# Kernel optimization log

Measured on AMD Instinct MI355X. Metric: run time of the kernel, lower is better.

The kernel has to match this reference:

```python
import jax, jax.numpy as jnp
import numpy as np

K_NEIGHBORS = 3  # self.K in DSVDD


def setup_inputs() -> dict:
    key = jax.random.key(0)
    k1, k2 = jax.random.split(key)
    B, N, C = 16, 3136, 112   # batch, h*w patches, descriptor channels
    M = 3136                  # memory-bank size
    phi_p = jax.random.normal(k1, (B, N, C), dtype=jnp.float32)
    C_bank = jax.random.normal(k2, (C, M), dtype=jnp.float32)
    return {"phi_p": phi_p, "C_bank": C_bank, "h": 56}


def reference(phi_p, C_bank, h):
    # squared distances via ||phi||^2 + ||c||^2 - 2 phi.c  -> (B, N, M)
    features = jnp.sum(phi_p * phi_p, axis=2, keepdims=True)        # (B, N, 1)
    centers = jnp.sum(C_bank * C_bank, axis=0, keepdims=True)       # (1, M)
    f_c = 2.0 * jnp.einsum('bnc,cm->bnm', phi_p, C_bank)            # (B, N, M)
    dist = jnp.sqrt(features + centers - f_c)                        # (B, N, M)
    # K smallest distances (ascending, like torch.topk(largest=False))
    neg_topk, _ = jax.lax.top_k(-dist, K_NEIGHBORS)                  # (B, N, K)
    dist_k = -neg_topk
    # softmin over K, take weight of the nearest neighbor times its distance
    softmin0 = jax.nn.softmax(-dist_k, axis=-1)[:, :, 0]             # (B, N)
    score = softmin0 * dist_k[:, :, 0]                               # (B, N)
    B, N = score.shape
    w = N // h
    return score.reshape(B, 1, h, w)  # b c h w with c=1
```

## Files before the change

kernel.cpp:

```cpp
#include <hip/hip_runtime.h>
#include <stdint.h>


typedef short s16x8 __attribute__((ext_vector_type(8)));
typedef float fx4 __attribute__((ext_vector_type(4)));

#define M_TOT 3136
#define CC 112
#define NROWS 50176
#define N_TILES_TOT 50

__device__ __forceinline__ unsigned short f2bf(float x) {
  unsigned u = __float_as_uint(x);
  u += 0x7fffu + ((u >> 16) & 1u);
  return (unsigned short)(u >> 16);
}

__device__ __forceinline__ void async16(const void* g, void* l) {
  __builtin_amdgcn_global_load_lds(
      (const __attribute__((address_space(1))) unsigned int*)g,
      (__attribute__((address_space(3))) unsigned int*)l, 16, 0, 0);
}

#define INSERT3(T0, T1, T2, V)                                  \
  do {                                                          \
    const float _a0 = (T0), _a1 = (T1), _v = (V);               \
    (T0) = fmaxf(_a0, _v);                                      \
    (T1) = __builtin_amdgcn_fmed3f(_a0, _a1, _v);               \
    (T2) = __builtin_amdgcn_fmed3f(_a1, (T2), _v);              \
  } while (0)

__global__ __launch_bounds__(256) void dsvdd_prep0(const float* __restrict__ Cb,
                                                   float* __restrict__ c2g) {
  const int m = blockIdx.x * 256 + threadIdx.x;
  if (m >= 3200) return;
  float ss = 20000.0f;
  if (m < M_TOT) {
    ss = 0.f;
    for (int k = 0; k < CC; ++k) {
      const float x = Cb[(size_t)k * M_TOT + m];
      ss += x * x;
    }
  }
  c2g[m] = ss;
}

__global__ __launch_bounds__(256) void dsvdd_prep1(const float* __restrict__ Cb,
                                                   const float* __restrict__ c2g,
                                                   unsigned char* __restrict__ CT2) {
  const int tile = blockIdx.x;
#pragma unroll
  for (int it = 0; it < 4; ++it) {
    const int s = it * 256 + threadIdx.x;
    const int f = s >> 8;
    const int ks = (s >> 6) & 3;
    const int l = s & 63;
    const int mm = tile * 64 + f * 16 + (l & 15);
    const bool mv = (mm < M_TOT);
    const int k0 = ks * 32 + (l >> 4) * 8;
    float v[8];
#pragma unroll
    for (int j = 0; j < 8; ++j) {
      const int k = k0 + j;
      float x = 0.f;
      if (k < CC) x = mv ? Cb[(size_t)k * M_TOT + mm] : 0.f;
      else if (k < 116) x = -0.125f * c2g[mm];
      v[j] = x;
    }
    uint4 pk;
    pk.x = (unsigned)f2bf(v[0]) | ((unsigned)f2bf(v[1]) << 16);
    pk.y = (unsigned)f2bf(v[2]) | ((unsigned)f2bf(v[3]) << 16);
    pk.z = (unsigned)f2bf(v[4]) | ((unsigned)f2bf(v[5]) << 16);
    pk.w = (unsigned)f2bf(v[6]) | ((unsigned)f2bf(v[7]) << 16);
    *(uint4*)(CT2 + (size_t)tile * 16384 + (size_t)s * 16) = pk;
  }
}

__global__ __launch_bounds__(256, 2) void dsvdd_stage1(const float* __restrict__ phi,
                                                       const unsigned char* __restrict__ CT2,
                                                       float* __restrict__ part,
                                                       float* __restrict__ featg, int nT) {
  __shared__ __align__(16) unsigned char lds[49152];

  const int t = threadIdx.x;
  const int lane = t & 63;
  const int w = t >> 6;
  const int g = w >> 1;
  const int h = w & 1;
  const int cq = lane & 15;
  const int kq = lane >> 4;
  const int c = blockIdx.y;
  const int tile0 = c * nT;
  const long rowBase = (long)blockIdx.x * 128;

#define STAGE(OFF, TIDX)                                                          \
  do {                                                                            \
    const unsigned char* _g =                                                     \
        CT2 + (size_t)(TIDX)*16384 + (size_t)w * 4096 + (size_t)lane * 16;        \
    unsigned char* _l = lds + (OFF) + w * 4096;                                   \
    _Pragma("unroll") for (int ii = 0; ii < 4; ++ii)                              \
        async16(_g + ii * 1024, _l + ii * 1024);                                  \
  } while (0)

  s16x8 bg[4][4];
  float ssr[4];
#pragma unroll
  for (int pf = 0; pf < 4; ++pf) {
    ssr[pf] = 0.f;
    const float* rp = phi + (size_t)(rowBase + g * 64 + pf * 16 + cq) * CC;
#pragma unroll
    for (int ks = 0; ks < 4; ++ks) {
      const int k0 = ks * 32 + kq * 8;
      s16x8 v;
      if (k0 <= 104) {
        const float4 a = *(const float4*)(rp + k0);
        const float4 b = *(const float4*)(rp + k0 + 4);
        ssr[pf] += a.x * a.x + a.y * a.y + a.z * a.z + a.w * a.w;
        ssr[pf] += b.x * b.x + b.y * b.y + b.z * b.z + b.w * b.w;
        v[0] = (short)f2bf(a.x); v[1] = (short)f2bf(a.y);
        v[2] = (short)f2bf(a.z); v[3] = (short)f2bf(a.w);
        v[4] = (short)f2bf(b.x); v[5] = (short)f2bf(b.y);
        v[6] = (short)f2bf(b.z); v[7] = (short)f2bf(b.w);
      } else if (k0 == 112) {
        v[0] = v[1] = v[2] = v[3] = (short)0x3f80;
        v[4] = v[5] = v[6] = v[7] = 0;
      } else {
        v = (s16x8)0;
      }
      bg[ks][pf] = v;
    }
    ssr[pf] += __shfl_xor(ssr[pf], 16);
    ssr[pf] += __shfl_xor(ssr[pf], 32);
  }

  STAGE(0, tile0 + 0);
  STAGE(16384, tile0 + 1);

  if (c == 0 && kq == 0) {
#pragma unroll
    for (int pf = 0; pf < 4; ++pf)
      featg[rowBase + g * 64 + pf * 16 + cq] = ssr[pf];
  }

  float t0[4], t1[4], t2[4];
#pragma unroll
  for (int pf = 0; pf < 4; ++pf) t0[pf] = t1[pf] = t2[pf] = -3.0e38f;

  int rd_off = 0;
  for (int tt = 0; tt < nT; ++tt) {
    if (tt + 1 < nT) {
      asm volatile("s_waitcnt vmcnt(4)" ::: "memory");
    } else {
      asm volatile("s_waitcnt vmcnt(0)" ::: "memory");
    }
    __builtin_amdgcn_s_barrier();
    __builtin_amdgcn_sched_barrier(0);
    if (tt + 2 < nT) {
      int wr = rd_off + 32768;
      if (wr >= 49152) wr -= 49152;
      STAGE(wr, tile0 + tt + 2);
    }
    const unsigned char* rd = lds + rd_off;
#pragma unroll
    for (int mf = 0; mf < 2; ++mf) {
      const int f = h * 2 + mf;
      s16x8 af[4];
#pragma unroll
      for (int ks = 0; ks < 4; ++ks)
        af[ks] = *(const s16x8*)(rd + (f * 4 + ks) * 1024 + lane * 16);
      fx4 acc[4];
      const fx4 zz = {0.f, 0.f, 0.f, 0.f};
#pragma unroll
      for (int ks = 0; ks < 4; ++ks)
#pragma unroll
        for (int pf = 0; pf < 4; ++pf)
          acc[pf] = __builtin_amdgcn_mfma_f32_16x16x32_bf16(
              af[ks], bg[ks][pf], (ks == 0) ? zz : acc[pf], 0, 0, 0);
#pragma unroll
      for (int pf = 0; pf < 4; ++pf)
#pragma unroll
        for (int rg = 0; rg < 4; ++rg)
          INSERT3(t0[pf], t1[pf], t2[pf], acc[pf][rg]);
    }
    rd_off += 16384;
    if (rd_off == 49152) rd_off = 0;
  }
#undef STAGE

#pragma unroll
  for (int pf = 0; pf < 4; ++pf) {
#pragma unroll
    for (int off = 16; off < 64; off <<= 1) {
      const float b0 = __shfl_xor(t0[pf], off);
      const float b1 = __shfl_xor(t1[pf], off);
      const float b2 = __shfl_xor(t2[pf], off);
      INSERT3(t0[pf], t1[pf], t2[pf], b0);
      INSERT3(t0[pf], t1[pf], t2[pf], b1);
      INSERT3(t0[pf], t1[pf], t2[pf], b2);
    }
  }
  __syncthreads();
  float(*const mg)[8] = (float(*)[8])lds;
  if (kq == 0) {
#pragma unroll
    for (int pf = 0; pf < 4; ++pf) {
      const int row = g * 64 + pf * 16 + cq;
      mg[row][h * 3 + 0] = t0[pf];
      mg[row][h * 3 + 1] = t1[pf];
      mg[row][h * 3 + 2] = t2[pf];
    }
  }
  __syncthreads();
  if (t < 128) {
    float s0 = mg[t][0], s1 = mg[t][1], s2 = mg[t][2];
    INSERT3(s0, s1, s2, mg[t][3]);
    INSERT3(s0, s1, s2, mg[t][4]);
    INSERT3(s0, s1, s2, mg[t][5]);
    float* dst = part + ((size_t)c * NROWS + rowBase + t) * 3;
    dst[0] = s0; dst[1] = s1; dst[2] = s2;
  }
}

__global__ __launch_bounds__(256) void dsvdd_stage2(const float* __restrict__ part,
                                                    const float* __restrict__ featg,
                                                    float* __restrict__ out, int S) {
  const int row = blockIdx.x * 256 + threadIdx.x;
  if (row >= NROWS) return;
  float s0 = -3.0e38f, s1 = -3.0e38f, s2 = -3.0e38f;
  for (int c = 0; c < S; ++c) {
    const float* p = part + ((size_t)c * NROWS + row) * 3;
    INSERT3(s0, s1, s2, p[0]);
    INSERT3(s0, s1, s2, p[1]);
    INSERT3(s0, s1, s2, p[2]);
  }
  const float feat = featg[row];
  const float d0 = sqrtf(fmaxf(feat - 2.f * s0, 0.f));
  const float d1 = sqrtf(fmaxf(feat - 2.f * s1, 0.f));
  const float d2 = sqrtf(fmaxf(feat - 2.f * s2, 0.f));
  const float w0 = 1.0f / (1.0f + __expf(d0 - d1) + __expf(d0 - d2));
  out[row] = w0 * d0;
}

extern "C" void kernel_launch(void* const* d_in, const int* in_sizes, int n_in,
                              void* d_out, int out_size, void* d_ws, size_t ws_size,
                              hipStream_t stream) {
  (void)in_sizes; (void)n_in; (void)out_size;
  const float* phi = (const float*)d_in[0];
  const float* Cb = (const float*)d_in[1];
  float* out = (float*)d_out;
  unsigned char* CT2 = (unsigned char*)d_ws;
  float* c2g = (float*)((unsigned char*)d_ws + 819200);
  float* featg = (float*)((unsigned char*)d_ws + 832000);
  float* partp = (float*)((unsigned char*)d_ws + 832000 + 200704);
  const size_t base = 832000 + 200704;
  int S = 1;
  if (ws_size >= base + (size_t)5 * NROWS * 12) S = 5;
  else if (ws_size >= base + (size_t)2 * NROWS * 12) S = 2;
  const int nT = N_TILES_TOT / S;
  dsvdd_prep0<<<13, 256, 0, stream>>>(Cb, c2g);
  dsvdd_prep1<<<50, 256, 0, stream>>>(Cb, c2g, CT2);
  dsvdd_stage1<<<dim3(392, S), 256, 0, stream>>>(phi, CT2, partp, featg, nT);
  dsvdd_stage2<<<196, 256, 0, stream>>>(partp, featg, out, S);
}
```

Baseline: 76.65 us.

## Load bank tiles directly to registers and fuse prep kernels

Removes the LDS triple-buffered async staging of bank tiles and instead has each wave load its A fragments straight from global memory into registers, double-buffered across iterations, with no barriers. The two prep kernels are merged into one that computes the column norms with an in-block reduction, and the feature-norm computation is skipped for non-zero splits. This drops the block-wide barrier per tile and cuts LDS use, which could raise occupancy. In exchange it relies on L2/L1 for reuse of the shared tile across the four waves and adds register pressure.

```diff
diff --git a/kernel.cpp b/kernel.cpp
--- a/kernel.cpp
+++ b/kernel.cpp
@@ -14,12 +14,6 @@
   unsigned u = __float_as_uint(x);
   u += 0x7fffu + ((u >> 16) & 1u);
   return (unsigned short)(u >> 16);
-}
-
-__device__ __forceinline__ void async16(const void* g, void* l) {
-  __builtin_amdgcn_global_load_lds(
-      (const __attribute__((address_space(1))) unsigned int*)g,
-      (__attribute__((address_space(3))) unsigned int*)l, 16, 0, 0);
 }
 
 #define INSERT3(T0, T1, T2, V)                                  \
@@ -30,32 +24,36 @@
     (T2) = __builtin_amdgcn_fmed3f(_a1, (T2), _v);              \
   } while (0)
 
-__global__ __launch_bounds__(256) void dsvdd_prep0(const float* __restrict__ Cb,
-                                                   float* __restrict__ c2g) {
-  const int m = blockIdx.x * 256 + threadIdx.x;
-  if (m >= 3200) return;
-  float ss = 20000.0f;
+__global__ __launch_bounds__(256) void dsvdd_prep(const float* __restrict__ Cb,
+                                                  unsigned char* __restrict__ CT2) {
+  const int tile = blockIdx.x;
+  __shared__ float partial[256];
+  __shared__ float c2s[64];
+  const int tm = threadIdx.x & 63;
+  const int seg = threadIdx.x >> 6;
+  const int m = tile * 64 + tm;
+  float ss = 0.f;
   if (m < M_TOT) {
-    ss = 0.f;
-    for (int k = 0; k < CC; ++k) {
+    for (int k = seg * 28; k < seg * 28 + 28; ++k) {
       const float x = Cb[(size_t)k * M_TOT + m];
       ss += x * x;
     }
   }
-  c2g[m] = ss;
-}
-
-__global__ __launch_bounds__(256) void dsvdd_prep1(const float* __restrict__ Cb,
-                                                   const float* __restrict__ c2g,
-                                                   unsigned char* __restrict__ CT2) {
-  const int tile = blockIdx.x;
+  partial[threadIdx.x] = ss;
+  __syncthreads();
+  if (seg == 0) {
+    const float c2 = partial[tm] + partial[64 + tm] + partial[128 + tm] + partial[192 + tm];
+    c2s[tm] = (m < M_TOT) ? (-0.125f * c2) : -2500.0f;
+  }
+  __syncthreads();
 #pragma unroll
   for (int it = 0; it < 4; ++it) {
     const int s = it * 256 + threadIdx.x;
     const int f = s >> 8;
     const int ks = (s >> 6) & 3;
     const int l = s & 63;
-    const int mm = tile * 64 + f * 16 + (l & 15);
+    const int mloc = f * 16 + (l & 15);
+    const int mm = tile * 64 + mloc;
     const bool mv = (mm < M_TOT);
     const int k0 = ks * 32 + (l >> 4) * 8;
     float v[8];
@@ -64,7 +62,7 @@
       const int k = k0 + j;
       float x = 0.f;
       if (k < CC) x = mv ? Cb[(size_t)k * M_TOT + mm] : 0.f;
-      else if (k < 116) x = -0.125f * c2g[mm];
+      else if (k < 116) x = c2s[mloc];
       v[j] = x;
     }
     uint4 pk;
@@ -80,7 +78,7 @@
                                                        const unsigned char* __restrict__ CT2,
                                                        float* __restrict__ part,
                                                        float* __restrict__ featg, int nT) {
-  __shared__ __align__(16) unsigned char lds[49152];
+  __shared__ float mg[128][8];
 
   const int t = threadIdx.x;
   const int lane = t & 63;
@@ -92,15 +90,7 @@
   const int c = blockIdx.y;
   const int tile0 = c * nT;
   const long rowBase = (long)blockIdx.x * 128;
-
-#define STAGE(OFF, TIDX)                                                          \
-  do {                                                                            \
-    const unsigned char* _g =                                                     \
-        CT2 + (size_t)(TIDX)*16384 + (size_t)w * 4096 + (size_t)lane * 16;        \
-    unsigned char* _l = lds + (OFF) + w * 4096;                                   \
-    _Pragma("unroll") for (int ii = 0; ii < 4; ++ii)                              \
-        async16(_g + ii * 1024, _l + ii * 1024);                                  \
-  } while (0)
+  const bool needF = (c == 0);
 
   s16x8 bg[4][4];
   float ssr[4];
@@ -115,8 +105,10 @@
       if (k0 <= 104) {
         const float4 a = *(const float4*)(rp + k0);
         const float4 b = *(const float4*)(rp + k0 + 4);
-        ssr[pf] += a.x * a.x + a.y * a.y + a.z * a.z + a.w * a.w;
-        ssr[pf] += b.x * b.x + b.y * b.y + b.z * b.z + b.w * b.w;
+        if (needF) {
+          ssr[pf] += a.x * a.x + a.y * a.y + a.z * a.z + a.w * a.w;
+          ssr[pf] += b.x * b.x + b.y * b.y + b.z * b.z + b.w * b.w;
+        }
         v[0] = (short)f2bf(a.x); v[1] = (short)f2bf(a.y);
         v[2] = (short)f2bf(a.z); v[3] = (short)f2bf(a.w);
         v[4] = (short)f2bf(b.x); v[5] = (short)f2bf(b.y);
@@ -129,14 +121,12 @@
       }
       bg[ks][pf] = v;
     }
-    ssr[pf] += __shfl_xor(ssr[pf], 16);
-    ssr[pf] += __shfl_xor(ssr[pf], 32);
-  }
-
-  STAGE(0, tile0 + 0);
-  STAGE(16384, tile0 + 1);
-
-  if (c == 0 && kq == 0) {
+    if (needF) {
+      ssr[pf] += __shfl_xor(ssr[pf], 16);
+      ssr[pf] += __shfl_xor(ssr[pf], 32);
+    }
+  }
+  if (needF && kq == 0) {
 #pragma unroll
     for (int pf = 0; pf < 4; ++pf)
       featg[rowBase + g * 64 + pf * 16 + cq] = ssr[pf];
@@ -146,46 +136,51 @@
 #pragma unroll
   for (int pf = 0; pf < 4; ++pf) t0[pf] = t1[pf] = t2[pf] = -3.0e38f;
 
-  int rd_off = 0;
-  for (int tt = 0; tt < nT; ++tt) {
-    if (tt + 1 < nT) {
-      asm volatile("s_waitcnt vmcnt(4)" ::: "memory");
-    } else {
-      asm volatile("s_waitcnt vmcnt(0)" ::: "memory");
-    }
-    __builtin_amdgcn_s_barrier();
-    __builtin_amdgcn_sched_barrier(0);
-    if (tt + 2 < nT) {
-      int wr = rd_off + 32768;
-      if (wr >= 49152) wr -= 49152;
-      STAGE(wr, tile0 + tt + 2);
-    }
-    const unsigned char* rd = lds + rd_off;
-#pragma unroll
-    for (int mf = 0; mf < 2; ++mf) {
-      const int f = h * 2 + mf;
-      s16x8 af[4];
-#pragma unroll
-      for (int ks = 0; ks < 4; ++ks)
-        af[ks] = *(const s16x8*)(rd + (f * 4 + ks) * 1024 + lane * 16);
-      fx4 acc[4];
-      const fx4 zz = {0.f, 0.f, 0.f, 0.f};
-#pragma unroll
-      for (int ks = 0; ks < 4; ++ks)
-#pragma unroll
-        for (int pf = 0; pf < 4; ++pf)
-          acc[pf] = __builtin_amdgcn_mfma_f32_16x16x32_bf16(
-              af[ks], bg[ks][pf], (ks == 0) ? zz : acc[pf], 0, 0, 0);
-#pragma unroll
-      for (int pf = 0; pf < 4; ++pf)
-#pragma unroll
-        for (int rg = 0; rg < 4; ++rg)
-          INSERT3(t0[pf], t1[pf], t2[pf], acc[pf][rg]);
-    }
-    rd_off += 16384;
-    if (rd_off == 49152) rd_off = 0;
-  }
-#undef STAGE
+  const unsigned char* ap = CT2 + (size_t)(h * 2) * 4096 + (size_t)lane * 16;
+  s16x8 afA[8], afB[8];
+
+#define LOADAF(DST, TIDX)                                                     \
+  do {                                                                        \
+    const unsigned char* _p = ap + (size_t)(TIDX)*16384;                      \
+    _Pragma("unroll") for (int mf = 0; mf < 2; ++mf)                          \
+        _Pragma("unroll") for (int ks = 0; ks < 4; ++ks)                      \
+            DST[mf * 4 + ks] = *(const s16x8*)(_p + mf * 4096 + ks * 1024);   \
+  } while (0)
+
+#define COMPUTE(SRC)                                                          \
+  do {                                                                        \
+    const fx4 _zz = {0.f, 0.f, 0.f, 0.f};                                     \
+    _Pragma("unroll") for (int mf = 0; mf < 2; ++mf) {                        \
+      fx4 acc[4];                                                             \
+      _Pragma("unroll") for (int ks = 0; ks < 4; ++ks)                        \
+          _Pragma("unroll") for (int pf = 0; pf < 4; ++pf)                    \
+              acc[pf] = __builtin_amdgcn_mfma_f32_16x16x32_bf16(              \
+                  SRC[mf * 4 + ks], bg[ks][pf], (ks == 0) ? _zz : acc[pf],    \
+                  0, 0, 0);                                                   \
+      _Pragma("unroll") for (int pf = 0; pf < 4; ++pf)                        \
+          _Pragma("unroll") for (int rg = 0; rg < 4; ++rg)                    \
+              INSERT3(t0[pf], t1[pf], t2[pf], acc[pf][rg]);                   \
+    }                                                                         \
+  } while (0)
+
+  LOADAF(afA, tile0);
+  int tt = 0;
+  while (tt + 2 < nT) {
+    LOADAF(afB, tile0 + tt + 1);
+    COMPUTE(afA);
+    LOADAF(afA, tile0 + tt + 2);
+    COMPUTE(afB);
+    tt += 2;
+  }
+  if (tt + 1 < nT) {
+    LOADAF(afB, tile0 + tt + 1);
+    COMPUTE(afA);
+    COMPUTE(afB);
+  } else {
+    COMPUTE(afA);
+  }
+#undef LOADAF
+#undef COMPUTE
 
 #pragma unroll
   for (int pf = 0; pf < 4; ++pf) {
@@ -199,8 +194,6 @@
       INSERT3(t0[pf], t1[pf], t2[pf], b2);
     }
   }
-  __syncthreads();
-  float(*const mg)[8] = (float(*)[8])lds;
   if (kq == 0) {
 #pragma unroll
     for (int pf = 0; pf < 4; ++pf) {
@@ -249,16 +242,14 @@
   const float* Cb = (const float*)d_in[1];
   float* out = (float*)d_out;
   unsigned char* CT2 = (unsigned char*)d_ws;
-  float* c2g = (float*)((unsigned char*)d_ws + 819200);
-  float* featg = (float*)((unsigned char*)d_ws + 832000);
-  float* partp = (float*)((unsigned char*)d_ws + 832000 + 200704);
-  const size_t base = 832000 + 200704;
+  float* featg = (float*)((unsigned char*)d_ws + 819200);
+  float* partp = (float*)((unsigned char*)d_ws + 819200 + 200704);
+  const size_t base = 819200 + 200704;
   int S = 1;
   if (ws_size >= base + (size_t)5 * NROWS * 12) S = 5;
   else if (ws_size >= base + (size_t)2 * NROWS * 12) S = 2;
   const int nT = N_TILES_TOT / S;
-  dsvdd_prep0<<<13, 256, 0, stream>>>(Cb, c2g);
-  dsvdd_prep1<<<50, 256, 0, stream>>>(Cb, c2g, CT2);
+  dsvdd_prep<<<50, 256, 0, stream>>>(Cb, CT2);
   dsvdd_stage1<<<dim3(392, S), 256, 0, stream>>>(phi, CT2, partp, featg, nT);
   dsvdd_stage2<<<196, 256, 0, stream>>>(partp, featg, out, S);
 }
```

Result: faster. 64.28 us (-16.1%).

## Double rows per block and stage whole bank chunk into 128KB LDS

Applied to the files above, without the earlier changes.

Stage1 now uses 512-thread blocks covering 256 rows each, so every staged memory-bank tile is reused by twice as many rows. The 10-tile chunk is loaded into a 128KB LDS buffer with a fixed three-phase load/compute schedule in place of the rolling triple buffer. Other changes: the chunk count is fixed at 5 instead of depending on workspace size, prep1 runs as 200 blocks, the -c²/8 fold is precomputed in prep0, and the feature norms are computed only by the c==0 blocks. The large LDS footprint and bigger blocks lower occupancy, and the kernel now assumes the workspace is large enough.

```diff
diff --git a/kernel.cpp b/kernel.cpp
--- a/kernel.cpp
+++ b/kernel.cpp
@@ -8,7 +8,8 @@
 #define M_TOT 3136
 #define CC 112
 #define NROWS 50176
-#define N_TILES_TOT 50
+#define NT 10
+#define S_CHUNKS 5
 
 __device__ __forceinline__ unsigned short f2bf(float x) {
   unsigned u = __float_as_uint(x);
@@ -31,56 +32,56 @@
   } while (0)
 
 __global__ __launch_bounds__(256) void dsvdd_prep0(const float* __restrict__ Cb,
-                                                   float* __restrict__ c2g) {
+                                                   float* __restrict__ foldv) {
   const int m = blockIdx.x * 256 + threadIdx.x;
   if (m >= 3200) return;
-  float ss = 20000.0f;
+  float r = -2500.0f;
   if (m < M_TOT) {
-    ss = 0.f;
+    float ss = 0.f;
     for (int k = 0; k < CC; ++k) {
       const float x = Cb[(size_t)k * M_TOT + m];
       ss += x * x;
     }
-  }
-  c2g[m] = ss;
+    r = -0.125f * ss;
+  }
+  foldv[m] = r;
 }
 
 __global__ __launch_bounds__(256) void dsvdd_prep1(const float* __restrict__ Cb,
-                                                   const float* __restrict__ c2g,
+                                                   const float* __restrict__ foldv,
                                                    unsigned char* __restrict__ CT2) {
-  const int tile = blockIdx.x;
-#pragma unroll
-  for (int it = 0; it < 4; ++it) {
-    const int s = it * 256 + threadIdx.x;
-    const int f = s >> 8;
-    const int ks = (s >> 6) & 3;
-    const int l = s & 63;
-    const int mm = tile * 64 + f * 16 + (l & 15);
-    const bool mv = (mm < M_TOT);
-    const int k0 = ks * 32 + (l >> 4) * 8;
-    float v[8];
-#pragma unroll
-    for (int j = 0; j < 8; ++j) {
-      const int k = k0 + j;
-      float x = 0.f;
-      if (k < CC) x = mv ? Cb[(size_t)k * M_TOT + mm] : 0.f;
-      else if (k < 116) x = -0.125f * c2g[mm];
-      v[j] = x;
-    }
-    uint4 pk;
-    pk.x = (unsigned)f2bf(v[0]) | ((unsigned)f2bf(v[1]) << 16);
-    pk.y = (unsigned)f2bf(v[2]) | ((unsigned)f2bf(v[3]) << 16);
-    pk.z = (unsigned)f2bf(v[4]) | ((unsigned)f2bf(v[5]) << 16);
-    pk.w = (unsigned)f2bf(v[6]) | ((unsigned)f2bf(v[7]) << 16);
-    *(uint4*)(CT2 + (size_t)tile * 16384 + (size_t)s * 16) = pk;
-  }
-}
-
-__global__ __launch_bounds__(256, 2) void dsvdd_stage1(const float* __restrict__ phi,
+  const int tile = blockIdx.x >> 2;
+  const int s = (blockIdx.x & 3) * 256 + threadIdx.x;
+  const int f = s >> 8;
+  const int ks = (s >> 6) & 3;
+  const int l = s & 63;
+  const int mm = tile * 64 + f * 16 + (l & 15);
+  const bool mv = (mm < M_TOT);
+  const int k0 = ks * 32 + (l >> 4) * 8;
+  const float fv = foldv[mm];
+  float v[8];
+#pragma unroll
+  for (int j = 0; j < 8; ++j) {
+    const int k = k0 + j;
+    float x = 0.f;
+    if (k < CC) x = mv ? Cb[(size_t)k * M_TOT + mm] : 0.f;
+    else if (k < 116) x = fv;
+    v[j] = x;
+  }
+  uint4 pk;
+  pk.x = (unsigned)f2bf(v[0]) | ((unsigned)f2bf(v[1]) << 16);
+  pk.y = (unsigned)f2bf(v[2]) | ((unsigned)f2bf(v[3]) << 16);
+  pk.z = (unsigned)f2bf(v[4]) | ((unsigned)f2bf(v[5]) << 16);
+  pk.w = (unsigned)f2bf(v[6]) | ((unsigned)f2bf(v[7]) << 16);
+  *(uint4*)(CT2 + (size_t)tile * 16384 + (size_t)s * 16) = pk;
+}
+
+__global__ __launch_bounds__(512, 2) void dsvdd_stage1(const float* __restrict__ phi,
                                                        const unsigned char* __restrict__ CT2,
                                                        float* __restrict__ part,
-                                                       float* __restrict__ featg, int nT) {
-  __shared__ __align__(16) unsigned char lds[49152];
+                                                       float* __restrict__ featg) {
+  __shared__ __align__(16) unsigned char lds[131072];
+  float(*const mg)[8] = (float(*)[8])lds;
 
   const int t = threadIdx.x;
   const int lane = t & 63;
@@ -90,17 +91,9 @@
   const int cq = lane & 15;
   const int kq = lane >> 4;
   const int c = blockIdx.y;
-  const int tile0 = c * nT;
-  const long rowBase = (long)blockIdx.x * 128;
-
-#define STAGE(OFF, TIDX)                                                          \
-  do {                                                                            \
-    const unsigned char* _g =                                                     \
-        CT2 + (size_t)(TIDX)*16384 + (size_t)w * 4096 + (size_t)lane * 16;        \
-    unsigned char* _l = lds + (OFF) + w * 4096;                                   \
-    _Pragma("unroll") for (int ii = 0; ii < 4; ++ii)                              \
-        async16(_g + ii * 1024, _l + ii * 1024);                                  \
-  } while (0)
+  const size_t chunkB = (size_t)c * (NT * 16384);
+  const long rowBase = (long)blockIdx.x * 256;
+  const bool needF = (c == 0);
 
   s16x8 bg[4][4];
   float ssr[4];
@@ -115,8 +108,10 @@
       if (k0 <= 104) {
         const float4 a = *(const float4*)(rp + k0);
         const float4 b = *(const float4*)(rp + k0 + 4);
-        ssr[pf] += a.x * a.x + a.y * a.y + a.z * a.z + a.w * a.w;
-        ssr[pf] += b.x * b.x + b.y * b.y + b.z * b.z + b.w * b.w;
+        if (needF) {
+          ssr[pf] += a.x * a.x + a.y * a.y + a.z * a.z + a.w * a.w;
+          ssr[pf] += b.x * b.x + b.y * b.y + b.z * b.z + b.w * b.w;
+        }
         v[0] = (short)f2bf(a.x); v[1] = (short)f2bf(a.y);
         v[2] = (short)f2bf(a.z); v[3] = (short)f2bf(a.w);
         v[4] = (short)f2bf(b.x); v[5] = (short)f2bf(b.y);
@@ -129,14 +124,12 @@
       }
       bg[ks][pf] = v;
     }
-    ssr[pf] += __shfl_xor(ssr[pf], 16);
-    ssr[pf] += __shfl_xor(ssr[pf], 32);
-  }
-
-  STAGE(0, tile0 + 0);
-  STAGE(16384, tile0 + 1);
-
-  if (c == 0 && kq == 0) {
+    if (needF) {
+      ssr[pf] += __shfl_xor(ssr[pf], 16);
+      ssr[pf] += __shfl_xor(ssr[pf], 32);
+    }
+  }
+  if (needF && h == 0 && kq == 0) {
 #pragma unroll
     for (int pf = 0; pf < 4; ++pf)
       featg[rowBase + g * 64 + pf * 16 + cq] = ssr[pf];
@@ -146,46 +139,71 @@
 #pragma unroll
   for (int pf = 0; pf < 4; ++pf) t0[pf] = t1[pf] = t2[pf] = -3.0e38f;
 
-  int rd_off = 0;
-  for (int tt = 0; tt < nT; ++tt) {
-    if (tt + 1 < nT) {
-      asm volatile("s_waitcnt vmcnt(4)" ::: "memory");
-    } else {
-      asm volatile("s_waitcnt vmcnt(0)" ::: "memory");
-    }
-    __builtin_amdgcn_s_barrier();
-    __builtin_amdgcn_sched_barrier(0);
-    if (tt + 2 < nT) {
-      int wr = rd_off + 32768;
-      if (wr >= 49152) wr -= 49152;
-      STAGE(wr, tile0 + tt + 2);
-    }
-    const unsigned char* rd = lds + rd_off;
-#pragma unroll
-    for (int mf = 0; mf < 2; ++mf) {
-      const int f = h * 2 + mf;
-      s16x8 af[4];
-#pragma unroll
-      for (int ks = 0; ks < 4; ++ks)
-        af[ks] = *(const s16x8*)(rd + (f * 4 + ks) * 1024 + lane * 16);
-      fx4 acc[4];
-      const fx4 zz = {0.f, 0.f, 0.f, 0.f};
-#pragma unroll
-      for (int ks = 0; ks < 4; ++ks)
-#pragma unroll
-        for (int pf = 0; pf < 4; ++pf)
-          acc[pf] = __builtin_amdgcn_mfma_f32_16x16x32_bf16(
-              af[ks], bg[ks][pf], (ks == 0) ? zz : acc[pf], 0, 0, 0);
-#pragma unroll
-      for (int pf = 0; pf < 4; ++pf)
-#pragma unroll
-        for (int rg = 0; rg < 4; ++rg)
-          INSERT3(t0[pf], t1[pf], t2[pf], acc[pf][rg]);
-    }
-    rd_off += 16384;
-    if (rd_off == 49152) rd_off = 0;
-  }
-#undef STAGE
+#define ISSUE(LDSOFF, CHOFF, PERW, NI)                                          \
+  do {                                                                          \
+    const unsigned char* _g = CT2 + chunkB + (CHOFF) + w * (PERW) + (size_t)lane * 16; \
+    unsigned char* _l = lds + (LDSOFF) + w * (PERW);                            \
+    _Pragma("unroll") for (int i = 0; i < (NI); ++i)                            \
+        async16(_g + i * 1024, _l + i * 1024);                                  \
+  } while (0)
+
+#define COMPUTE(RD)                                                             \
+  do {                                                                          \
+    const unsigned char* _rd = (RD);                                            \
+    const fx4 _zz = {0.f, 0.f, 0.f, 0.f};                                       \
+    _Pragma("unroll") for (int mf = 0; mf < 2; ++mf) {                          \
+      s16x8 af[4];                                                              \
+      _Pragma("unroll") for (int ks = 0; ks < 4; ++ks)                          \
+          af[ks] = *(const s16x8*)(_rd + ((h * 2 + mf) * 4 + ks) * 1024 +       \
+                                   lane * 16);                                  \
+      fx4 acc[4];                                                               \
+      _Pragma("unroll") for (int ks = 0; ks < 4; ++ks)                          \
+          _Pragma("unroll") for (int pf = 0; pf < 4; ++pf)                      \
+              acc[pf] = __builtin_amdgcn_mfma_f32_16x16x32_bf16(                \
+                  af[ks], bg[ks][pf], (ks == 0) ? _zz : acc[pf], 0, 0, 0);      \
+      _Pragma("unroll") for (int pf = 0; pf < 4; ++pf)                          \
+          _Pragma("unroll") for (int rg = 0; rg < 4; ++rg)                      \
+              INSERT3(t0[pf], t1[pf], t2[pf], acc[pf][rg]);                     \
+    }                                                                           \
+  } while (0)
+
+#define FENCE() __builtin_amdgcn_sched_barrier(0)
+
+  ISSUE(0, 0, 8192, 8);
+  ISSUE(65536, 65536, 8192, 8);
+  FENCE();
+  asm volatile("s_waitcnt vmcnt(8)" ::: "memory");
+  FENCE();
+  __builtin_amdgcn_s_barrier();
+  FENCE();
+  COMPUTE(lds + 0 * 16384);
+  COMPUTE(lds + 1 * 16384);
+  COMPUTE(lds + 2 * 16384);
+  COMPUTE(lds + 3 * 16384);
+  FENCE();
+  __builtin_amdgcn_s_barrier();
+  FENCE();
+  ISSUE(0, 131072, 4096, 4);
+  FENCE();
+  asm volatile("s_waitcnt vmcnt(4)" ::: "memory");
+  FENCE();
+  __builtin_amdgcn_s_barrier();
+  FENCE();
+  COMPUTE(lds + 65536 + 0 * 16384);
+  COMPUTE(lds + 65536 + 1 * 16384);
+  COMPUTE(lds + 65536 + 2 * 16384);
+  COMPUTE(lds + 65536 + 3 * 16384);
+  FENCE();
+  asm volatile("s_waitcnt vmcnt(0)" ::: "memory");
+  FENCE();
+  __builtin_amdgcn_s_barrier();
+  FENCE();
+  COMPUTE(lds + 0 * 16384);
+  COMPUTE(lds + 1 * 16384);
+
+#undef ISSUE
+#undef COMPUTE
+#undef FENCE
 
 #pragma unroll
   for (int pf = 0; pf < 4; ++pf) {
@@ -200,7 +218,6 @@
     }
   }
   __syncthreads();
-  float(*const mg)[8] = (float(*)[8])lds;
   if (kq == 0) {
 #pragma unroll
     for (int pf = 0; pf < 4; ++pf) {
@@ -211,7 +228,7 @@
     }
   }
   __syncthreads();
-  if (t < 128) {
+  if (t < 256) {
     float s0 = mg[t][0], s1 = mg[t][1], s2 = mg[t][2];
     INSERT3(s0, s1, s2, mg[t][3]);
     INSERT3(s0, s1, s2, mg[t][4]);
@@ -223,11 +240,12 @@
 
 __global__ __launch_bounds__(256) void dsvdd_stage2(const float* __restrict__ part,
                                                     const float* __restrict__ featg,
-                                                    float* __restrict__ out, int S) {
+                                                    float* __restrict__ out) {
   const int row = blockIdx.x * 256 + threadIdx.x;
   if (row >= NROWS) return;
   float s0 = -3.0e38f, s1 = -3.0e38f, s2 = -3.0e38f;
-  for (int c = 0; c < S; ++c) {
+#pragma unroll
+  for (int c = 0; c < S_CHUNKS; ++c) {
     const float* p = part + ((size_t)c * NROWS + row) * 3;
     INSERT3(s0, s1, s2, p[0]);
     INSERT3(s0, s1, s2, p[1]);
@@ -244,21 +262,16 @@
 extern "C" void kernel_launch(void* const* d_in, const int* in_sizes, int n_in,
                               void* d_out, int out_size, void* d_ws, size_t ws_size,
                               hipStream_t stream) {
-  (void)in_sizes; (void)n_in; (void)out_size;
+  (void)in_sizes; (void)n_in; (void)out_size; (void)ws_size;
   const float* phi = (const float*)d_in[0];
   const float* Cb = (const float*)d_in[1];
   float* out = (float*)d_out;
   unsigned char* CT2 = (unsigned char*)d_ws;
-  float* c2g = (float*)((unsigned char*)d_ws + 819200);
+  float* foldv = (float*)((unsigned char*)d_ws + 819200);
   float* featg = (float*)((unsigned char*)d_ws + 832000);
-  float* partp = (float*)((unsigned char*)d_ws + 832000 + 200704);
-  const size_t base = 832000 + 200704;
-  int S = 1;
-  if (ws_size >= base + (size_t)5 * NROWS * 12) S = 5;
-  else if (ws_size >= base + (size_t)2 * NROWS * 12) S = 2;
-  const int nT = N_TILES_TOT / S;
-  dsvdd_prep0<<<13, 256, 0, stream>>>(Cb, c2g);
-  dsvdd_prep1<<<50, 256, 0, stream>>>(Cb, c2g, CT2);
-  dsvdd_stage1<<<dim3(392, S), 256, 0, stream>>>(phi, CT2, partp, featg, nT);
-  dsvdd_stage2<<<196, 256, 0, stream>>>(partp, featg, out, S);
-}
+  float* partp = (float*)((unsigned char*)d_ws + 1032704);
+  dsvdd_prep0<<<13, 256, 0, stream>>>(Cb, foldv);
+  dsvdd_prep1<<<200, 256, 0, stream>>>(Cb, foldv, CT2);
+  dsvdd_stage1<<<dim3(196, S_CHUNKS), 512, 0, stream>>>(phi, CT2, partp, featg);
+  dsvdd_stage2<<<196, 256, 0, stream>>>(partp, featg, out);
+}
```

Result: slower. 79.10 us (+3.2%).
